# Performance work log

Hardware: AMD Instinct MI355X
Metric: run time of the kernel (lower is better)

The kernel has to match this reference:

```python
import jax, jax.numpy as jnp
import numpy as np

B, T, F, N = 262144, 3, 17, 8
EMBD = 32
DT = 0.2  # 25/5*0.04
EPS = 1e-8  # torch.cosine_similarity eps


def _mono(x, wi, bi, wo, bo):
    # monotonic_fun with increasing=False: relu(-Linear(x)) -> Linear
    h = jax.nn.relu(-(x @ wi.T + bi))  # (..., EMBD)
    return h @ wo.T + bo               # (..., 1)


def _cos(a, b):
    dot = jnp.sum(a * b, axis=-1)
    na = jnp.maximum(jnp.linalg.norm(a, axis=-1), EPS)
    nb = jnp.maximum(jnp.linalg.norm(b, axis=-1), EPS)
    return dot / (na * nb)


def _angle_clamp(vec, e, ang):
    # vec: (B,K,2), e: (B,2) -> keep forces within effective angle cone, sum over K
    keep = jnp.abs(_cos(e[:, None, :], vec)) > ang
    return jnp.sum(vec * keep[..., None], axis=1)


def setup_inputs() -> dict:
    key = jax.random.key(0)
    ks = jax.random.split(key, 8)
    ego = jax.random.normal(ks[0], (B, T, F), jnp.float32)
    ego = ego.at[:, :, 2:4].multiply(10.0)  # position scale
    nei = jax.random.normal(ks[1], (B, N, F), jnp.float32)
    nei = nei.at[:, :, 2:4].multiply(10.0).at[:, :, 4:6].multiply(0.1)
    border = jax.random.normal(ks[2], (4,), jnp.float32)
    attr_dest_para = jax.random.uniform(ks[3], (2,), jnp.float32) + 0.1  # relu(rand), keep away from 0 divisor
    eff_angle = jax.nn.sigmoid(jax.random.uniform(ks[4], (1,), jnp.float32))

    def mlp(k):
        k1, k2, k3, k4 = jax.random.split(k, 4)
        wi = jax.random.uniform(k1, (EMBD, 1), jnp.float32)      # clamped >= 0
        bi = jax.random.normal(k2, (EMBD,), jnp.float32) * 0.1
        wo = jax.random.uniform(k3, (1, EMBD), jnp.float32) * 0.1  # clamped >= 0
        bo = jax.random.normal(k4, (1,), jnp.float32) * 0.1
        return wi, bi, wo, bo

    an = mlp(ks[5])
    rn = mlp(ks[6])
    rb = mlp(ks[7])
    dl = mlp(jax.random.fold_in(key, 99))
    return dict(
        ego=ego, nei=nei, border=border,
        attr_dest_para=attr_dest_para, eff_angle=eff_angle,
        an_wi=an[0], an_bi=an[1], an_wo=an[2], an_bo=an[3],
        rn_wi=rn[0], rn_bi=rn[1], rn_wo=rn[2], rn_bo=rn[3],
        rb_wi=rb[0], rb_bi=rb[1], rb_wo=rb[2], rb_bo=rb[3],
        dl_wi=dl[0], dl_bi=dl[1], dl_wo=dl[2], dl_bo=dl[3],
    )


def reference(ego, nei, border, attr_dest_para, eff_angle,
              an_wi, an_bi, an_wo, an_bo,
              rn_wi, rn_bi, rn_wo, rn_bo,
              rb_wi, rb_bi, rb_wo, rb_bo,
              dl_wi, dl_bi, dl_wo, dl_bo):
    ego_last = ego[:, -1]  # (B,F)

    # --- attr_destination (desired_velocity=None branch) ---
    v34 = ego_last[:, 3:5]
    dv = jnp.stack([jnp.linalg.norm(v34, axis=-1),
                    jnp.zeros(ego.shape[0], ego.dtype)], axis=1)  # (B,2)
    f_dest = ((attr_dest_para[1] * dv - v34) / attr_dest_para[0])[:, None, :]  # (B,1,2)

    # --- attr_repu_neighbors ---
    r = nei[:, :, 2:4] - ego_last[:, None, 2:4]  # (B,N,2)
    mask = nei[:, :, 2:4] == 0                    # (B,N,2)
    r_norm = jnp.linalg.norm(r, axis=-1, keepdims=True)  # (B,N,1)

    # neighbor durality: quirky use of batch element 1, shared across batch
    ids_last = ego[1, -1, 8:-1]  # (8,) neighbor-id columns
    dur = jnp.zeros(N, ego.dtype)
    for t in range(ego.shape[1]):
        dur = dur + jnp.isin(ids_last, ego[1, t, 8:-1]).astype(ego.dtype)

    f_attr = _mono(r_norm, an_wi, an_bi, an_wo, an_bo) * r / r_norm \
             * _mono(dur[:, None], dl_wi, dl_bi, dl_wo, dl_bo)  # (B,N,2)*(N,1)
    f_attr = jnp.where(mask, 0.0, f_attr)

    v_nei = nei[:, :, 4:6]
    b = r_norm \
        + jnp.sum((r + v_nei * DT) ** 2, axis=-1, keepdims=True) \
        - jnp.sum((v_nei * DT) ** 2, axis=-1, keepdims=True)
    b = jnp.sqrt(b) / 2
    f_repu = _mono(b, rn_wi, rn_bi, rn_wo, rn_bo) * r / r_norm
    f_repu = jnp.where(mask, 0.0, f_repu)

    # --- repu_borders (select_lane = [0, -1]) ---
    rb_all = ego_last[:, 3, None] - border        # (B,4)
    rbv = jnp.stack([rb_all[:, 0], rb_all[:, -1]], axis=1)  # (B,2)
    rbn = jnp.abs(rbv)
    f_bor = _mono(rbn[..., None], rb_wi, rb_bi, rb_wo, rb_bo) * (rbv / rbn)[..., None]  # (B,2,1)
    f_bor = jnp.concatenate([jnp.zeros_like(f_bor), f_bor], axis=-1)  # (B,2,2): [0, fy]

    # --- angle clamp + integrate ---
    e = ego_last[:, 4:6]
    e = e / jnp.linalg.norm(e, axis=1, keepdims=True)
    a = (_angle_clamp(f_dest, e, eff_angle)
         + _angle_clamp(f_attr, e, eff_angle) + _angle_clamp(f_repu, e, eff_angle)
         + _angle_clamp(f_bor, e, eff_angle))
    v = ego_last[:, 2:4] + a * DT
    s = ego_last[:, :2] + v * DT
    return jnp.concatenate([s, v, a], axis=1)  # (B,6)
```

## Files before the change

kernel.cpp:

```cpp
#include <hip/hip_runtime.h>

#define DTC 0.2f
#define EPSC 1e-8f

__global__ void sfm_pre(const float* __restrict__ ego,
                        const float* __restrict__ dl_wi,
                        const float* __restrict__ dl_bi,
                        const float* __restrict__ dl_wo,
                        const float* __restrict__ dl_bo,
                        float* __restrict__ ws) {
    int j = threadIdx.x;
    if (j >= 8) return;
    const float* base = ego + 51;
    float idv = base[2 * 17 + 8 + j];
    float dur = 0.f;
    for (int t = 0; t < 3; ++t) {
        bool found = false;
        for (int m = 0; m < 8; ++m) found = found || (idv == base[t * 17 + 8 + m]);
        dur += found ? 1.f : 0.f;
    }
    float acc = 0.f;
    for (int k = 0; k < 32; ++k) {
        float h = fmaxf(0.f, -(dl_wi[k] * dur + dl_bi[k]));
        acc = fmaf(dl_wo[k], h, acc);
    }
    ws[j] = acc + dl_bo[0];
}

__global__ __launch_bounds__(256) void sfm_main(
    const float* __restrict__ ego, const float* __restrict__ nei,
    const float* __restrict__ border, const float* __restrict__ adp,
    const float* __restrict__ eang,
    const float* __restrict__ an_wi, const float* __restrict__ an_bi,
    const float* __restrict__ an_wo, const float* __restrict__ an_bo,
    const float* __restrict__ rn_wi, const float* __restrict__ rn_bi,
    const float* __restrict__ rn_wo, const float* __restrict__ rn_bo,
    const float* __restrict__ rb_wi, const float* __restrict__ rb_bi,
    const float* __restrict__ rb_wo, const float* __restrict__ rb_bo,
    const float* __restrict__ dlf,
    float* __restrict__ out, int Bn)
{
    __shared__ float sw[9 * 32 + 16];
    int t = threadIdx.x;
    if (t < 32) {
        sw[t]        = an_wi[t]; sw[32 + t]  = an_bi[t]; sw[64 + t]  = an_wo[t];
        sw[96 + t]   = rn_wi[t]; sw[128 + t] = rn_bi[t]; sw[160 + t] = rn_wo[t];
        sw[192 + t]  = rb_wi[t]; sw[224 + t] = rb_bi[t]; sw[256 + t] = rb_wo[t];
    }
    if (t >= 32 && t < 40) sw[288 + (t - 32)] = dlf[t - 32];
    if (t == 40) sw[296] = an_bo[0];
    if (t == 41) sw[297] = rn_bo[0];
    if (t == 42) sw[298] = rb_bo[0];
    if (t == 43) sw[299] = adp[0];
    if (t == 44) sw[300] = adp[1];
    if (t == 45) sw[301] = eang[0];
    if (t == 46) sw[302] = border[0];
    if (t == 47) sw[303] = border[3];
    __syncthreads();

    int b = blockIdx.x * 256 + t;
    if (b >= Bn) return;

    const float* eg = ego + (long long)b * 51 + 34;
    float g0 = eg[0], g1 = eg[1], g2 = eg[2], g3 = eg[3], g4 = eg[4], g5 = eg[5];

    float rx[8], ry[8], rno[8], bb[8], mfx[8], mfy[8];
    const float* nb = nei + (long long)b * 136 + 2;
#pragma unroll
    for (int j = 0; j < 8; ++j) {
        float nx = nb[j * 17 + 0];
        float ny = nb[j * 17 + 1];
        float vx = nb[j * 17 + 2];
        float vy = nb[j * 17 + 3];
        mfx[j] = (nx == 0.f) ? 0.f : 1.f;
        mfy[j] = (ny == 0.f) ? 0.f : 1.f;
        float Rx = nx - g2, Ry = ny - g3;
        rx[j] = Rx; ry[j] = Ry;
        float rr = sqrtf(Rx * Rx + Ry * Ry);
        rno[j] = rr;
        float ax = fmaf(vx, DTC, Rx), ay = fmaf(vy, DTC, Ry);
        float wx = vx * DTC, wy = vy * DTC;
        float bval = rr + (ax * ax + ay * ay) - (wx * wx + wy * wy);
        bb[j] = sqrtf(bval) * 0.5f;
    }

    float accA[8], accR[8];
#pragma unroll
    for (int j = 0; j < 8; ++j) { accA[j] = 0.f; accR[j] = 0.f; }
    float rb0 = g3 - sw[302], rb1 = g3 - sw[303];
    float rbn0 = fabsf(rb0), rbn1 = fabsf(rb1);
    float accB0 = 0.f, accB1 = 0.f;
#pragma unroll 4
    for (int k = 0; k < 32; ++k) {
        float awi = sw[k],       abi  = sw[32 + k],  awo = sw[64 + k];
        float rwi = sw[96 + k],  rbi  = sw[128 + k], rwo = sw[160 + k];
        float bwi = sw[192 + k], bbi2 = sw[224 + k], bwo = sw[256 + k];
#pragma unroll
        for (int j = 0; j < 8; ++j) {
            float h = fmaxf(0.f, -fmaf(awi, rno[j], abi));
            accA[j] = fmaf(awo, h, accA[j]);
            float g = fmaxf(0.f, -fmaf(rwi, bb[j], rbi));
            accR[j] = fmaf(rwo, g, accR[j]);
        }
        float h0 = fmaxf(0.f, -fmaf(bwi, rbn0, bbi2)); accB0 = fmaf(bwo, h0, accB0);
        float h1 = fmaxf(0.f, -fmaf(bwi, rbn1, bbi2)); accB1 = fmaf(bwo, h1, accB1);
    }

    float an_bo_v = sw[296], rn_bo_v = sw[297], rb_bo_v = sw[298];
    float p0 = sw[299], p1 = sw[300], ang = sw[301];

    float elen = sqrtf(g4 * g4 + g5 * g5);
    float ex = g4 / elen, ey = g5 / elen;
    float na = fmaxf(sqrtf(ex * ex + ey * ey), EPSC);

    float axs = 0.f, ays = 0.f;
#define CLAMP_ADD(VX, VY)                                                   \
    {                                                                       \
        float _vx = (VX), _vy = (VY);                                       \
        float _nv = fmaxf(sqrtf(_vx * _vx + _vy * _vy), EPSC);              \
        float _c = (ex * _vx + ey * _vy) / (na * _nv);                      \
        if (fabsf(_c) > ang) { axs += _vx; ays += _vy; }                    \
    }

    {
        float dvn = sqrtf(g3 * g3 + g4 * g4);
        float fdx = (p1 * dvn - g3) / p0;
        float fdy = (0.f - g4) / p0;
        CLAMP_ADD(fdx, fdy);
    }
#pragma unroll
    for (int j = 0; j < 8; ++j) {
        float coef = (accA[j] + an_bo_v) / rno[j] * sw[288 + j];
        CLAMP_ADD(coef * rx[j] * mfx[j], coef * ry[j] * mfy[j]);
    }
#pragma unroll
    for (int j = 0; j < 8; ++j) {
        float coef = (accR[j] + rn_bo_v) / rno[j];
        CLAMP_ADD(coef * rx[j] * mfx[j], coef * ry[j] * mfy[j]);
    }
    {
        float f0 = (accB0 + rb_bo_v) * (rb0 / rbn0);
        float f1 = (accB1 + rb_bo_v) * (rb1 / rbn1);
        CLAMP_ADD(0.f, f0);
        CLAMP_ADD(0.f, f1);
    }
#undef CLAMP_ADD

    float vxo = fmaf(axs, DTC, g2);
    float vyo = fmaf(ays, DTC, g3);
    float sx  = fmaf(vxo, DTC, g0);
    float sy  = fmaf(vyo, DTC, g1);

    float* op = out + (long long)b * 6;
    op[0] = sx;  op[1] = sy;
    op[2] = vxo; op[3] = vyo;
    op[4] = axs; op[5] = ays;
}

extern "C" void kernel_launch(void* const* d_in, const int* in_sizes, int n_in,
                              void* d_out, int out_size, void* d_ws, size_t ws_size,
                              hipStream_t stream) {
    const float* ego    = (const float*)d_in[0];
    const float* nei    = (const float*)d_in[1];
    const float* border = (const float*)d_in[2];
    const float* adp    = (const float*)d_in[3];
    const float* eang   = (const float*)d_in[4];
    const float* an_wi  = (const float*)d_in[5];
    const float* an_bi  = (const float*)d_in[6];
    const float* an_wo  = (const float*)d_in[7];
    const float* an_bo  = (const float*)d_in[8];
    const float* rn_wi  = (const float*)d_in[9];
    const float* rn_bi  = (const float*)d_in[10];
    const float* rn_wo  = (const float*)d_in[11];
    const float* rn_bo  = (const float*)d_in[12];
    const float* rb_wi  = (const float*)d_in[13];
    const float* rb_bi  = (const float*)d_in[14];
    const float* rb_wo  = (const float*)d_in[15];
    const float* rb_bo  = (const float*)d_in[16];
    const float* dl_wi  = (const float*)d_in[17];
    const float* dl_bi  = (const float*)d_in[18];
    const float* dl_wo  = (const float*)d_in[19];
    const float* dl_bo  = (const float*)d_in[20];
    float* out = (float*)d_out;
    float* ws  = (float*)d_ws;

    int Bn = in_sizes[0] / (3 * 17);

    sfm_pre<<<1, 64, 0, stream>>>(ego, dl_wi, dl_bi, dl_wo, dl_bo, ws);

    int grid = (Bn + 255) / 256;
    sfm_main<<<grid, 256, 0, stream>>>(ego, nei, border, adp, eang,
                                       an_wi, an_bi, an_wo, an_bo,
                                       rn_wi, rn_bi, rn_wo, rn_bo,
                                       rb_wi, rb_bi, rb_wo, rb_bo,
                                       ws, out, Bn);
}
```

Measured before the change: 289.1 us.

## Assign one lane per neighbor and reduce forces with wavefront shuffles

```diff
diff --git a/kernel.cpp b/kernel.cpp
--- a/kernel.cpp
+++ b/kernel.cpp
@@ -9,22 +9,20 @@
                         const float* __restrict__ dl_wo,
                         const float* __restrict__ dl_bo,
                         float* __restrict__ ws) {
-    int j = threadIdx.x;
-    if (j >= 8) return;
+    int t = threadIdx.x;
+    int j = t >> 5, k = t & 31;
     const float* base = ego + 51;
     float idv = base[2 * 17 + 8 + j];
     float dur = 0.f;
-    for (int t = 0; t < 3; ++t) {
-        bool found = false;
-        for (int m = 0; m < 8; ++m) found = found || (idv == base[t * 17 + 8 + m]);
-        dur += found ? 1.f : 0.f;
+    for (int tt = 0; tt < 3; ++tt) {
+        bool f = false;
+        for (int m = 0; m < 8; ++m) f = f || (idv == base[tt * 17 + 8 + m]);
+        dur += f ? 1.f : 0.f;
     }
-    float acc = 0.f;
-    for (int k = 0; k < 32; ++k) {
-        float h = fmaxf(0.f, -(dl_wi[k] * dur + dl_bi[k]));
-        acc = fmaf(dl_wo[k], h, acc);
-    }
-    ws[j] = acc + dl_bo[0];
+    float part = dl_wo[k] * fmaxf(0.f, -fmaf(dl_wi[k], dur, dl_bi[k]));
+#pragma unroll
+    for (int m = 1; m < 32; m <<= 1) part += __shfl_xor(part, m, 64);
+    if (k == 0) ws[j] = part + dl_bo[0];
 }
 
 __global__ __launch_bounds__(256) void sfm_main(
@@ -40,7 +38,7 @@
     const float* __restrict__ dlf,
     float* __restrict__ out, int Bn)
 {
-    __shared__ float sw[9 * 32 + 16];
+    __shared__ float sw[304];
     int t = threadIdx.x;
     if (t < 32) {
         sw[t]        = an_wi[t]; sw[32 + t]  = an_bi[t]; sw[64 + t]  = an_wo[t];
@@ -58,52 +56,47 @@
     if (t == 47) sw[303] = border[3];
     __syncthreads();
 
-    int b = blockIdx.x * 256 + t;
-    if (b >= Bn) return;
+    int l = t & 7;
+    long long row = (long long)blockIdx.x * 32 + (t >> 3);
+    if (row >= Bn) return;
 
-    const float* eg = ego + (long long)b * 51 + 34;
-    float g0 = eg[0], g1 = eg[1], g2 = eg[2], g3 = eg[3], g4 = eg[4], g5 = eg[5];
+    float egv = 0.f;
+    if (l < 6) egv = ego[row * 51 + 34 + l];
+    int lb = (t & 63) & ~7;
+    float g0 = __shfl(egv, lb + 0, 64);
+    float g1 = __shfl(egv, lb + 1, 64);
+    float g2 = __shfl(egv, lb + 2, 64);
+    float g3 = __shfl(egv, lb + 3, 64);
+    float g4 = __shfl(egv, lb + 4, 64);
+    float g5 = __shfl(egv, lb + 5, 64);
 
-    float rx[8], ry[8], rno[8], bb[8], mfx[8], mfy[8];
-    const float* nb = nei + (long long)b * 136 + 2;
-#pragma unroll
-    for (int j = 0; j < 8; ++j) {
-        float nx = nb[j * 17 + 0];
-        float ny = nb[j * 17 + 1];
-        float vx = nb[j * 17 + 2];
-        float vy = nb[j * 17 + 3];
-        mfx[j] = (nx == 0.f) ? 0.f : 1.f;
-        mfy[j] = (ny == 0.f) ? 0.f : 1.f;
-        float Rx = nx - g2, Ry = ny - g3;
-        rx[j] = Rx; ry[j] = Ry;
-        float rr = sqrtf(Rx * Rx + Ry * Ry);
-        rno[j] = rr;
-        float ax = fmaf(vx, DTC, Rx), ay = fmaf(vy, DTC, Ry);
-        float wx = vx * DTC, wy = vy * DTC;
-        float bval = rr + (ax * ax + ay * ay) - (wx * wx + wy * wy);
-        bb[j] = sqrtf(bval) * 0.5f;
-    }
+    const float* nr = nei + row * 136 + l * 17 + 2;
+    float nx = nr[0], ny = nr[1], vx = nr[2], vy = nr[3];
 
-    float accA[8], accR[8];
-#pragma unroll
-    for (int j = 0; j < 8; ++j) { accA[j] = 0.f; accR[j] = 0.f; }
+    float Rx = nx - g2, Ry = ny - g3;
+    float rr = sqrtf(Rx * Rx + Ry * Ry);
+    float ax = fmaf(vx, DTC, Rx), ay = fmaf(vy, DTC, Ry);
+    float wx = vx * DTC, wy = vy * DTC;
+    float bb = sqrtf(rr + ax * ax + ay * ay - wx * wx - wy * wy) * 0.5f;
+
     float rb0 = g3 - sw[302], rb1 = g3 - sw[303];
     float rbn0 = fabsf(rb0), rbn1 = fabsf(rb1);
-    float accB0 = 0.f, accB1 = 0.f;
-#pragma unroll 4
+
+    float accA = 0.f, accR = 0.f;
+#pragma unroll 8
     for (int k = 0; k < 32; ++k) {
-        float awi = sw[k],       abi  = sw[32 + k],  awo = sw[64 + k];
-        float rwi = sw[96 + k],  rbi  = sw[128 + k], rwo = sw[160 + k];
-        float bwi = sw[192 + k], bbi2 = sw[224 + k], bwo = sw[256 + k];
+        float h = fmaxf(0.f, -fmaf(sw[k], rr, sw[32 + k]));
+        accA = fmaf(sw[64 + k], h, accA);
+        float g = fmaxf(0.f, -fmaf(sw[96 + k], bb, sw[128 + k]));
+        accR = fmaf(sw[160 + k], g, accR);
+    }
+    float pB0 = 0.f, pB1 = 0.f;
 #pragma unroll
-        for (int j = 0; j < 8; ++j) {
-            float h = fmaxf(0.f, -fmaf(awi, rno[j], abi));
-            accA[j] = fmaf(awo, h, accA[j]);
-            float g = fmaxf(0.f, -fmaf(rwi, bb[j], rbi));
-            accR[j] = fmaf(rwo, g, accR[j]);
-        }
-        float h0 = fmaxf(0.f, -fmaf(bwi, rbn0, bbi2)); accB0 = fmaf(bwo, h0, accB0);
-        float h1 = fmaxf(0.f, -fmaf(bwi, rbn1, bbi2)); accB1 = fmaf(bwo, h1, accB1);
+    for (int m = 0; m < 4; ++m) {
+        int k = l + 8 * m;
+        float bwi = sw[192 + k], bbi = sw[224 + k], bwo = sw[256 + k];
+        pB0 = fmaf(bwo, fmaxf(0.f, -fmaf(bwi, rbn0, bbi)), pB0);
+        pB1 = fmaf(bwo, fmaxf(0.f, -fmaf(bwi, rbn1, bbi)), pB1);
     }
 
     float an_bo_v = sw[296], rn_bo_v = sw[297], rb_bo_v = sw[298];
@@ -122,39 +115,43 @@
         if (fabsf(_c) > ang) { axs += _vx; ays += _vy; }                    \
     }
 
+    float mfx = (nx == 0.f) ? 0.f : 1.f;
+    float mfy = (ny == 0.f) ? 0.f : 1.f;
+
     {
-        float dvn = sqrtf(g3 * g3 + g4 * g4);
-        float fdx = (p1 * dvn - g3) / p0;
-        float fdy = (0.f - g4) / p0;
-        CLAMP_ADD(fdx, fdy);
-    }
-#pragma unroll
-    for (int j = 0; j < 8; ++j) {
-        float coef = (accA[j] + an_bo_v) / rno[j] * sw[288 + j];
-        CLAMP_ADD(coef * rx[j] * mfx[j], coef * ry[j] * mfy[j]);
-    }
-#pragma unroll
-    for (int j = 0; j < 8; ++j) {
-        float coef = (accR[j] + rn_bo_v) / rno[j];
-        CLAMP_ADD(coef * rx[j] * mfx[j], coef * ry[j] * mfy[j]);
+        float coef = (accA + an_bo_v) / rr * sw[288 + l];
+        CLAMP_ADD(coef * Rx * mfx, coef * Ry * mfy);
     }
     {
-        float f0 = (accB0 + rb_bo_v) * (rb0 / rbn0);
-        float f1 = (accB1 + rb_bo_v) * (rb1 / rbn1);
+        float coef = (accR + rn_bo_v) / rr;
+        CLAMP_ADD(coef * Rx * mfx, coef * Ry * mfy);
+    }
+
+#pragma unroll
+    for (int m = 1; m < 8; m <<= 1) {
+        axs += __shfl_xor(axs, m, 64);
+        ays += __shfl_xor(ays, m, 64);
+        pB0 += __shfl_xor(pB0, m, 64);
+        pB1 += __shfl_xor(pB1, m, 64);
+    }
+
+    if (l == 0) {
+        float dvn = sqrtf(g3 * g3 + g4 * g4);
+        CLAMP_ADD((p1 * dvn - g3) / p0, -g4 / p0);
+        float f0 = (pB0 + rb_bo_v) * (rb0 / rbn0);
+        float f1 = (pB1 + rb_bo_v) * (rb1 / rbn1);
         CLAMP_ADD(0.f, f0);
         CLAMP_ADD(0.f, f1);
+
+        float vxo = fmaf(axs, DTC, g2);
+        float vyo = fmaf(ays, DTC, g3);
+        float* op = out + row * 6;
+        op[0] = fmaf(vxo, DTC, g0);
+        op[1] = fmaf(vyo, DTC, g1);
+        op[2] = vxo; op[3] = vyo;
+        op[4] = axs; op[5] = ays;
     }
 #undef CLAMP_ADD
-
-    float vxo = fmaf(axs, DTC, g2);
-    float vyo = fmaf(ays, DTC, g3);
-    float sx  = fmaf(vxo, DTC, g0);
-    float sy  = fmaf(vyo, DTC, g1);
-
-    float* op = out + (long long)b * 6;
-    op[0] = sx;  op[1] = sy;
-    op[2] = vxo; op[3] = vyo;
-    op[4] = axs; op[5] = ays;
 }
 
 extern "C" void kernel_launch(void* const* d_in, const int* in_sizes, int n_in,
@@ -186,9 +183,9 @@
 
     int Bn = in_sizes[0] / (3 * 17);
 
-    sfm_pre<<<1, 64, 0, stream>>>(ego, dl_wi, dl_bi, dl_wo, dl_bo, ws);
+    sfm_pre<<<1, 256, 0, stream>>>(ego, dl_wi, dl_bi, dl_wo, dl_bo, ws);
 
-    int grid = (Bn + 255) / 256;
+    int grid = (Bn + 31) / 32;
     sfm_main<<<grid, 256, 0, stream>>>(ego, nei, border, adp, eang,
                                        an_wi, an_bi, an_wo, an_bo,
                                        rn_wi, rn_bi, rn_wo, rn_bo,
```

New measurement: 278.8 us. 3.6% less time.
